# Kernel tuning notes

Measured on AMD Instinct MI355X. Metric: run time of the kernel, lower is better.

The kernel has to match this reference:

```python
import jax, jax.numpy as jnp
import numpy as np

N_NODES = 50000
N_EDGES = 1_600_000
IN_DIM = 512
HIDDEN = 512
OUT_DIM = 128
K = 10
ALPHA = 0.1


def setup_inputs() -> dict:
    key = jax.random.key(0)
    ks = jax.random.split(key, 7)
    x = jax.random.normal(ks[0], (N_NODES, IN_DIM), dtype=jnp.float32)
    edge_index = jax.random.randint(ks[1], (2, N_EDGES), 0, N_NODES, dtype=jnp.int64)
    s_in = 1.0 / np.sqrt(IN_DIM)
    s_h = 1.0 / np.sqrt(HIDDEN)
    lin_in_w = jax.random.uniform(ks[2], (HIDDEN, IN_DIM), jnp.float32, -s_in, s_in)
    lin_in_b = jax.random.uniform(ks[3], (HIDDEN,), jnp.float32, -s_in, s_in)
    lin_out_w = jax.random.uniform(ks[4], (OUT_DIM, HIDDEN), jnp.float32, -s_h, s_h)
    lin_out_b = jax.random.uniform(ks[5], (OUT_DIM,), jnp.float32, -s_h, s_h)
    # GPR init: alpha*(1-alpha)^k, normalized
    w = np.array([ALPHA * (1 - ALPHA) ** k for k in range(K + 1)], dtype=np.float32)
    gpr_weights = jnp.asarray(w / w.sum())
    return {
        "x": x, "edge_index": edge_index,
        "lin_in_w": lin_in_w, "lin_in_b": lin_in_b,
        "lin_out_w": lin_out_w, "lin_out_b": lin_out_b,
        "gpr_weights": gpr_weights,
    }


def reference(x, edge_index, lin_in_w, lin_in_b, lin_out_w, lin_out_b, gpr_weights):
    n = x.shape[0]
    loops = jnp.arange(n, dtype=edge_index.dtype)
    row = jnp.concatenate([edge_index[0], loops])  # [E+n]
    col = jnp.concatenate([edge_index[1], loops])
    # degree over rows (edge_index_sl[0]), clamped to >=1
    deg = jax.ops.segment_sum(jnp.ones_like(row, dtype=x.dtype), row, num_segments=n)
    dis = jnp.clip(deg, 1.0) ** -0.5  # deg^-0.5, [n]

    h = jax.nn.relu(x @ lin_in_w.T + lin_in_b)  # [n, hidden] (dropout = identity in eval)
    w = jax.nn.softmax(gpr_weights)  # [K+1]

    def step(carry, wk):
        h_prop, acc = carry
        hs = h_prop * dis[:, None]
        h_prop = jax.ops.segment_sum(hs[col], row, num_segments=n) * dis[:, None]
        return (h_prop, acc + wk * h_prop), None

    (_, h_final), _ = jax.lax.scan(step, (h, w[0] * h), w[1:])
    return h_final @ lin_out_w.T + lin_out_b
```

## Files before the change

### kernel.cpp

```cpp
#include <hip/hip_runtime.h>


#define SLOTS 96
#define CAP 2688

typedef __attribute__((ext_vector_type(8))) short short8;
typedef __attribute__((ext_vector_type(4))) float f32x4;

__device__ inline ushort f2bf(float f) {
    uint x = __float_as_uint(f);
    return (ushort)((x + 0x7fffu + ((x >> 16) & 1u)) >> 16);
}
__device__ inline float bflo(uint u) { return __uint_as_float(u << 16); }
__device__ inline float bfhi(uint u) { return __uint_as_float(u & 0xffff0000u); }

__global__ void init_misc_kernel(int* __restrict__ bcur, int nbc,
                                 ushort* __restrict__ yAll, size_t ystride, int zrow) {
    int i = blockIdx.x * blockDim.x + threadIdx.x;
    int stride = gridDim.x * blockDim.x;
    for (int j = i; j < nbc; j += stride) bcur[j] = 0;
    for (int j = i; j < 11 * 128; j += stride) {
        int k = j >> 7, d = j & 127;
        yAll[(size_t)k * ystride + (size_t)zrow * 128 + d] = 0;
    }
}

__global__ void fill_u32_kernel(uint* __restrict__ p, uint v, int cnt) {
    int i = blockIdx.x * blockDim.x + threadIdx.x;
    int stride = gridDim.x * blockDim.x;
    for (; i < cnt; i += stride) p[i] = v;
}

__global__ void bucket_scatter_kernel(const int* __restrict__ row, const int* __restrict__ col,
                                      int* __restrict__ bcur, uint* __restrict__ bbuf, int E) {
    int i = blockIdx.x * blockDim.x + threadIdx.x;
    int stride = gridDim.x * blockDim.x;
    for (; i < E; i += stride) {
        int r = __builtin_nontemporal_load(&row[i]);
        int c = __builtin_nontemporal_load(&col[i]);
        int b = r >> 6;
        int pos = atomicAdd(&bcur[b * 16], 1);
        if (pos < CAP)
            bbuf[(size_t)b * CAP + pos] = ((uint)(r & 63) << 16) | (uint)c;
    }
}

__global__ __launch_bounds__(256) void bucket_expand_kernel(
    const int* __restrict__ bcur, const uint* __restrict__ bbuf,
    ushort* __restrict__ col_s, int* __restrict__ deg,
    float* __restrict__ dis, float* __restrict__ dis2, float* __restrict__ rdis, int n) {
    __shared__ int cur[64];
    const int tid = threadIdx.x;
    const int b = blockIdx.x;
    if (tid < 64) cur[tid] = 0;
    __syncthreads();
    int cb = bcur[b * 16];
    if (cb > CAP) cb = CAP;
    const size_t bb = (size_t)b * CAP;
    for (int i = tid; i < cb; i += 256) {
        uint e = bbuf[bb + i];
        int rl = (int)(e >> 16);
        int pos = atomicAdd(&cur[rl], 1);
        if (pos < SLOTS)
            col_s[((size_t)(b * 64 + rl)) * SLOTS + pos] = (ushort)(e & 0xffffu);
    }
    __syncthreads();
    if (tid < 64) {
        int r = b * 64 + tid;
        if (r < n) {
            int d = cur[tid];
            deg[r] = d;
            float fd = (float)(d + 1);
            float di = rsqrtf(fd);
            dis[r] = di;
            dis2[r] = di * di;
            rdis[r] = sqrtf(fd);
        }
    }
}

__global__ void cvt_bf16_kernel(const float* __restrict__ in, ushort* __restrict__ out, int n4) {
    int i = blockIdx.x * blockDim.x + threadIdx.x;
    int stride = gridDim.x * blockDim.x;
    const float4* I = reinterpret_cast<const float4*>(in);
    ushort4* O = reinterpret_cast<ushort4*>(out);
    for (; i < n4; i += stride) {
        float4 v = I[i];
        ushort4 o;
        o.x = f2bf(v.x); o.y = f2bf(v.y); o.z = f2bf(v.z); o.w = f2bf(v.w);
        O[i] = o;
    }
}

template <int EPI>
__global__ __launch_bounds__(256) void gemm_mfma_kernel(
    const void* __restrict__ Ap, const ushort* __restrict__ B,
    const float* __restrict__ bias, const float* __restrict__ dis,
    ushort* __restrict__ outH, int M, int N, int K) {
    __shared__ __align__(16) short As[128 * 32];
    __shared__ __align__(16) short Bs[128 * 32];
    const int tid = threadIdx.x;
    const int lane = tid & 63;
    const int wv = tid >> 6;
    const int wm = (wv >> 1) * 64;
    const int wn = (wv & 1) * 64;
    const int bm = blockIdx.y * 128;
    const int bn = blockIdx.x * 128;
    const int lrow = lane & 15;
    const int lk8 = (lane >> 4) * 8;

    f32x4 acc[4][4];
#pragma unroll
    for (int i = 0; i < 4; ++i)
#pragma unroll
        for (int j = 0; j < 4; ++j) acc[i][j] = (f32x4)(0.f);

    const int r0 = tid >> 2;
    const int g0 = (tid & 3) * 8;

    for (int k0 = 0; k0 < K; k0 += 32) {
        short8 a0, a1;
        if (EPI == 0) {
            const float* Af = (const float*)Ap;
            float4 f0 = make_float4(0.f, 0.f, 0.f, 0.f), f1 = f0, f2 = f0, f3 = f0;
            if (bm + r0 < M) {
                f0 = *reinterpret_cast<const float4*>(Af + (size_t)(bm + r0) * K + k0 + g0);
                f1 = *reinterpret_cast<const float4*>(Af + (size_t)(bm + r0) * K + k0 + g0 + 4);
            }
            if (bm + r0 + 64 < M) {
                f2 = *reinterpret_cast<const float4*>(Af + (size_t)(bm + r0 + 64) * K + k0 + g0);
                f3 = *reinterpret_cast<const float4*>(Af + (size_t)(bm + r0 + 64) * K + k0 + g0 + 4);
            }
            a0[0] = (short)f2bf(f0.x); a0[1] = (short)f2bf(f0.y);
            a0[2] = (short)f2bf(f0.z); a0[3] = (short)f2bf(f0.w);
            a0[4] = (short)f2bf(f1.x); a0[5] = (short)f2bf(f1.y);
            a0[6] = (short)f2bf(f1.z); a0[7] = (short)f2bf(f1.w);
            a1[0] = (short)f2bf(f2.x); a1[1] = (short)f2bf(f2.y);
            a1[2] = (short)f2bf(f2.z); a1[3] = (short)f2bf(f2.w);
            a1[4] = (short)f2bf(f3.x); a1[5] = (short)f2bf(f3.y);
            a1[6] = (short)f2bf(f3.z); a1[7] = (short)f2bf(f3.w);
        } else {
            const ushort* Ab = (const ushort*)Ap;
            a0 = *reinterpret_cast<const short8*>(Ab + (size_t)(bm + r0) * K + k0 + g0);
            a1 = *reinterpret_cast<const short8*>(Ab + (size_t)(bm + r0 + 64) * K + k0 + g0);
        }
        short8 b0 = *reinterpret_cast<const short8*>(B + (size_t)(bn + r0) * K + k0 + g0);
        short8 b1 = *reinterpret_cast<const short8*>(B + (size_t)(bn + r0 + 64) * K + k0 + g0);
        __syncthreads();
        *reinterpret_cast<short8*>(As + r0 * 32 + g0) = a0;
        *reinterpret_cast<short8*>(As + (r0 + 64) * 32 + g0) = a1;
        *reinterpret_cast<short8*>(Bs + r0 * 32 + g0) = b0;
        *reinterpret_cast<short8*>(Bs + (r0 + 64) * 32 + g0) = b1;
        __syncthreads();
        short8 af[4], bfr[4];
#pragma unroll
        for (int mf = 0; mf < 4; ++mf)
            af[mf] = *reinterpret_cast<const short8*>(As + (wm + mf * 16 + lrow) * 32 + lk8);
#pragma unroll
        for (int nf = 0; nf < 4; ++nf)
            bfr[nf] = *reinterpret_cast<const short8*>(Bs + (wn + nf * 16 + lrow) * 32 + lk8);
#pragma unroll
        for (int mf = 0; mf < 4; ++mf)
#pragma unroll
            for (int nf = 0; nf < 4; ++nf)
                acc[mf][nf] = __builtin_amdgcn_mfma_f32_16x16x32_bf16(af[mf], bfr[nf], acc[mf][nf], 0, 0, 0);
    }

#pragma unroll
    for (int mf = 0; mf < 4; ++mf) {
#pragma unroll
        for (int nf = 0; nf < 4; ++nf) {
            const int col = bn + wn + nf * 16 + lrow;
#pragma unroll
            for (int r = 0; r < 4; ++r) {
                const int row = bm + wm + mf * 16 + (lane >> 4) * 4 + r;
                if (row < M) {
                    float v = acc[mf][nf][r];
                    if (EPI == 0) {
                        v = fmaxf(v + bias[col], 0.f);
                        outH[(size_t)row * N + col] = f2bf(v);
                    } else {
                        outH[(size_t)row * N + col] = f2bf(dis[row] * v);
                    }
                }
            }
        }
    }
}

__global__ __launch_bounds__(256) void spmm128_kernel(
    const int* __restrict__ deg, const ushort* __restrict__ col_s,
    const float* __restrict__ dis2,
    const ushort* __restrict__ y_old, ushort* __restrict__ y_new, int n) {
    int wid = (blockIdx.x * 256 + threadIdx.x) >> 6;
    if (wid >= n) return;
    wid = __builtin_amdgcn_readfirstlane(wid);
    const int lane = threadIdx.x & 63;
    int cnt = deg[wid];
    if (cnt > SLOTS) cnt = SLOTS;
    const int cnt16 = (cnt + 15) & ~15;
    const ushort* __restrict__ cp = col_s + (size_t)wid * SLOTS;
    const uint* __restrict__ Y = reinterpret_cast<const uint*>(y_old);
    float s0a = 0.f, s1a = 0.f, s0b = 0.f, s1b = 0.f;
    for (int t = 0; t < cnt16; t += 16) {
        int c[16];
        uint v[16];
#pragma unroll
        for (int j = 0; j < 16; ++j) c[j] = (int)cp[t + j];
#pragma unroll
        for (int j = 0; j < 16; ++j) v[j] = Y[(size_t)c[j] * 64 + lane];
#pragma unroll
        for (int j = 0; j < 16; ++j) {
            if (j & 1) { s0b += bflo(v[j]); s1b += bfhi(v[j]); }
            else       { s0a += bflo(v[j]); s1a += bfhi(v[j]); }
        }
    }
    const uint u = Y[(size_t)wid * 64 + lane];
    const float d2 = dis2[wid];
    const float y0 = d2 * (bflo(u) + (s0a + s0b));
    const float y1 = d2 * (bfhi(u) + (s1a + s1b));
    const uint pv = (uint)f2bf(y0) | ((uint)f2bf(y1) << 16);
    __builtin_nontemporal_store(pv, &reinterpret_cast<uint*>(y_new)[(size_t)wid * 64 + lane]);
}

__global__ __launch_bounds__(256) void finsum_kernel(
    const ushort* __restrict__ yAll, size_t ystride_dw,
    const float* __restrict__ gpr, const float* __restrict__ rdis,
    const float* __restrict__ bout, float* __restrict__ outp, int n) {
    __shared__ float w[11];
    if (threadIdx.x == 0) {
        float m = gpr[0];
        for (int i = 1; i < 11; ++i) m = fmaxf(m, gpr[i]);
        float e[11], s = 0.f;
        for (int i = 0; i < 11; ++i) { e[i] = expf(gpr[i] - m); s += e[i]; }
        float inv = 1.f / s;
        for (int i = 0; i < 11; ++i) w[i] = e[i] * inv;
    }
    __syncthreads();
    const int gid = blockIdx.x * 256 + threadIdx.x;
    if (gid >= n * 64) return;
    const int row = gid >> 6;
    const int lane = gid & 63;
    const uint* __restrict__ Y = reinterpret_cast<const uint*>(yAll);
    float s0 = 0.f, s1 = 0.f;
#pragma unroll
    for (int k = 0; k < 11; ++k) {
        const uint v = Y[k * ystride_dw + (size_t)row * 64 + lane];
        const float wk = w[k];
        s0 = fmaf(wk, bflo(v), s0);
        s1 = fmaf(wk, bfhi(v), s1);
    }
    const float r = rdis[row];
    float2 o;
    o.x = fmaf(s0, r, bout[lane * 2 + 0]);
    o.y = fmaf(s1, r, bout[lane * 2 + 1]);
    *reinterpret_cast<float2*>(outp + (size_t)row * 128 + lane * 2) = o;
}

extern "C" void kernel_launch(void* const* d_in, const int* in_sizes, int n_in,
                              void* d_out, int out_size, void* d_ws, size_t ws_size,
                              hipStream_t stream) {
    const float* x    = (const float*)d_in[0];
    const int*   ei   = (const int*)d_in[1];
    const float* win  = (const float*)d_in[2];
    const float* bin  = (const float*)d_in[3];
    const float* wout = (const float*)d_in[4];
    const float* bout = (const float*)d_in[5];
    const float* gpr  = (const float*)d_in[6];
    float* out = (float*)d_out;

    const int n = in_sizes[0] / 512;
    const int E = in_sizes[1] / 2;
    const int Mpad = ((n + 127) / 128) * 128;
    const int nb = (n + 63) >> 6;

    char* ws = (char*)d_ws;
    size_t off = 0;
    auto take = [&](size_t bytes) -> char* {
        char* p = ws + off;
        off += (bytes + 511) & ~(size_t)511;
        return p;
    };
    int*    deg     = (int*)take((size_t)n * sizeof(int));
    float*  dis     = (float*)take((size_t)n * sizeof(float));
    float*  dis2    = (float*)take((size_t)n * sizeof(float));
    float*  rdis    = (float*)take((size_t)n * sizeof(float));
    int*    bcur    = (int*)take((size_t)nb * 16 * sizeof(int));
    uint*   bbuf    = (uint*)take((size_t)nb * CAP * sizeof(uint));
    ushort* col_s   = (ushort*)take((size_t)n * SLOTS * sizeof(ushort));
    ushort* win_bf  = (ushort*)take((size_t)512 * 512 * sizeof(ushort));
    ushort* wout_bf = (ushort*)take((size_t)128 * 512 * sizeof(ushort));
    ushort* h_bf    = (ushort*)take((size_t)Mpad * 512 * sizeof(ushort));
    const size_t ystride = (size_t)Mpad * 128;
    ushort* yAll    = (ushort*)take(11 * ystride * sizeof(ushort));

    const int* rowp = ei;
    const int* colp = ei + E;

    init_misc_kernel<<<64, 256, 0, stream>>>(bcur, nb * 16, yAll, ystride, n);
    fill_u32_kernel<<<2048, 256, 0, stream>>>(
        (uint*)col_s, ((uint)n << 16) | (uint)n, n * SLOTS / 2);
    bucket_scatter_kernel<<<2048, 256, 0, stream>>>(rowp, colp, bcur, bbuf, E);
    bucket_expand_kernel<<<nb, 256, 0, stream>>>(bcur, bbuf, col_s, deg, dis, dis2, rdis, n);

    cvt_bf16_kernel<<<256, 256, 0, stream>>>(win, win_bf, 512 * 128);
    cvt_bf16_kernel<<<64, 256, 0, stream>>>(wout, wout_bf, 128 * 128);

    dim3 g1(4, Mpad / 128);
    gemm_mfma_kernel<0><<<g1, 256, 0, stream>>>(x, win_bf, bin, nullptr, h_bf, n, 512, 512);

    dim3 g2(1, Mpad / 128);
    gemm_mfma_kernel<2><<<g2, 256, 0, stream>>>(h_bf, wout_bf, nullptr, dis, yAll, n, 128, 512);

    const int spmm_blocks = (n + 3) / 4;
    for (int k = 1; k <= 10; ++k) {
        spmm128_kernel<<<spmm_blocks, 256, 0, stream>>>(
            deg, col_s, dis2, yAll + (size_t)(k - 1) * ystride, yAll + (size_t)k * ystride, n);
    }

    finsum_kernel<<<(n * 64 + 255) / 256, 256, 0, stream>>>(
        yAll, ystride / 2, gpr, rdis, bout, out, n);
}
```

Measured before the change: 738.1 us.

## Fuse weight bf16 conversion into GEMMs, merge init kernels, pad LDS, widen GEMM1 tile

Removes the separate bf16 conversion kernels for the weights; both GEMMs now read fp32 weights and convert them while staging into shared memory. The two init/fill kernels are merged into one launch. Shared-memory rows are padded from 32 to 36 shorts to cut bank conflicts on fragment loads. GEMM1 is split out with a 128x256 tile and 512 threads, which halves how often x is reloaded across N tiles, in exchange for converting the weights redundantly in every block.

Result: faster. 721.8 us (-2.2%).

```diff
diff --git a/kernel.cpp b/kernel.cpp
--- a/kernel.cpp
+++ b/kernel.cpp
@@ -3,6 +3,7 @@
 
 #define SLOTS 96
 #define CAP 2688
+#define LDP 36
 
 typedef __attribute__((ext_vector_type(8))) short short8;
 typedef __attribute__((ext_vector_type(4))) float f32x4;
@@ -14,21 +15,26 @@
 __device__ inline float bflo(uint u) { return __uint_as_float(u << 16); }
 __device__ inline float bfhi(uint u) { return __uint_as_float(u & 0xffff0000u); }
 
-__global__ void init_misc_kernel(int* __restrict__ bcur, int nbc,
-                                 ushort* __restrict__ yAll, size_t ystride, int zrow) {
-    int i = blockIdx.x * blockDim.x + threadIdx.x;
-    int stride = gridDim.x * blockDim.x;
-    for (int j = i; j < nbc; j += stride) bcur[j] = 0;
-    for (int j = i; j < 11 * 128; j += stride) {
-        int k = j >> 7, d = j & 127;
+__device__ inline short8 pack8(float4 a, float4 b) {
+    short8 o;
+    o[0] = (short)f2bf(a.x); o[1] = (short)f2bf(a.y);
+    o[2] = (short)f2bf(a.z); o[3] = (short)f2bf(a.w);
+    o[4] = (short)f2bf(b.x); o[5] = (short)f2bf(b.y);
+    o[6] = (short)f2bf(b.z); o[7] = (short)f2bf(b.w);
+    return o;
+}
+
+__global__ void init_kernel(int* __restrict__ bcur, int nbc,
+                            ushort* __restrict__ yAll, size_t ystride, int zrow,
+                            uint* __restrict__ cfill, int cfcnt, uint cfval) {
+    const int gid = blockIdx.x * blockDim.x + threadIdx.x;
+    const int stride = gridDim.x * blockDim.x;
+    for (int i = gid; i < cfcnt; i += stride) cfill[i] = cfval;
+    for (int i = gid; i < nbc; i += stride) bcur[i] = 0;
+    for (int i = gid; i < 11 * 128; i += stride) {
+        int k = i >> 7, d = i & 127;
         yAll[(size_t)k * ystride + (size_t)zrow * 128 + d] = 0;
     }
-}
-
-__global__ void fill_u32_kernel(uint* __restrict__ p, uint v, int cnt) {
-    int i = blockIdx.x * blockDim.x + threadIdx.x;
-    int stride = gridDim.x * blockDim.x;
-    for (; i < cnt; i += stride) p[i] = v;
 }
 
 __global__ void bucket_scatter_kernel(const int* __restrict__ row, const int* __restrict__ col,
@@ -79,33 +85,95 @@
     }
 }
 
-__global__ void cvt_bf16_kernel(const float* __restrict__ in, ushort* __restrict__ out, int n4) {
-    int i = blockIdx.x * blockDim.x + threadIdx.x;
-    int stride = gridDim.x * blockDim.x;
-    const float4* I = reinterpret_cast<const float4*>(in);
-    ushort4* O = reinterpret_cast<ushort4*>(out);
-    for (; i < n4; i += stride) {
-        float4 v = I[i];
-        ushort4 o;
-        o.x = f2bf(v.x); o.y = f2bf(v.y); o.z = f2bf(v.z); o.w = f2bf(v.w);
-        O[i] = o;
-    }
-}
-
-template <int EPI>
-__global__ __launch_bounds__(256) void gemm_mfma_kernel(
-    const void* __restrict__ Ap, const ushort* __restrict__ B,
-    const float* __restrict__ bias, const float* __restrict__ dis,
-    ushort* __restrict__ outH, int M, int N, int K) {
-    __shared__ __align__(16) short As[128 * 32];
-    __shared__ __align__(16) short Bs[128 * 32];
+__global__ __launch_bounds__(512) void gemm1_kernel(
+    const float* __restrict__ X, const float* __restrict__ Wf,
+    const float* __restrict__ bias, ushort* __restrict__ outH, int M) {
+    __shared__ __align__(16) short As[128 * LDP];
+    __shared__ __align__(16) short Bs[256 * LDP];
+    const int tid = threadIdx.x;
+    const int lane = tid & 63;
+    const int wv = tid >> 6;
+    const int wm = (wv >> 2) * 64;
+    const int wn = (wv & 3) * 64;
+    const int bm = blockIdx.y * 128;
+    const int bn = blockIdx.x * 256;
+    const int lrow = lane & 15;
+    const int lk8 = (lane >> 4) * 8;
+
+    f32x4 acc[4][4];
+#pragma unroll
+    for (int i = 0; i < 4; ++i)
+#pragma unroll
+        for (int j = 0; j < 4; ++j) acc[i][j] = (f32x4)(0.f);
+
+    const int ra = tid >> 2;
+    const int ga = (tid & 3) * 8;
+    const int rb = tid >> 1;
+    const int gb = (tid & 1) * 16;
+
+    for (int k0 = 0; k0 < 512; k0 += 32) {
+        float4 fz = make_float4(0.f, 0.f, 0.f, 0.f);
+        float4 f0 = fz, f1 = fz;
+        if (bm + ra < M) {
+            const float* xp = X + (size_t)(bm + ra) * 512 + k0 + ga;
+            f0 = *reinterpret_cast<const float4*>(xp);
+            f1 = *reinterpret_cast<const float4*>(xp + 4);
+        }
+        short8 av = pack8(f0, f1);
+        const float* wp = Wf + (size_t)(bn + rb) * 512 + k0 + gb;
+        float4 g0 = *reinterpret_cast<const float4*>(wp);
+        float4 g1 = *reinterpret_cast<const float4*>(wp + 4);
+        float4 g2 = *reinterpret_cast<const float4*>(wp + 8);
+        float4 g3 = *reinterpret_cast<const float4*>(wp + 12);
+        short8 bv0 = pack8(g0, g1);
+        short8 bv1 = pack8(g2, g3);
+        __syncthreads();
+        *reinterpret_cast<short8*>(As + ra * LDP + ga) = av;
+        *reinterpret_cast<short8*>(Bs + rb * LDP + gb) = bv0;
+        *reinterpret_cast<short8*>(Bs + rb * LDP + gb + 8) = bv1;
+        __syncthreads();
+        short8 af[4], bfr[4];
+#pragma unroll
+        for (int mf = 0; mf < 4; ++mf)
+            af[mf] = *reinterpret_cast<const short8*>(As + (wm + mf * 16 + lrow) * LDP + lk8);
+#pragma unroll
+        for (int nf = 0; nf < 4; ++nf)
+            bfr[nf] = *reinterpret_cast<const short8*>(Bs + (wn + nf * 16 + lrow) * LDP + lk8);
+#pragma unroll
+        for (int mf = 0; mf < 4; ++mf)
+#pragma unroll
+            for (int nf = 0; nf < 4; ++nf)
+                acc[mf][nf] = __builtin_amdgcn_mfma_f32_16x16x32_bf16(af[mf], bfr[nf], acc[mf][nf], 0, 0, 0);
+    }
+
+#pragma unroll
+    for (int mf = 0; mf < 4; ++mf) {
+#pragma unroll
+        for (int nf = 0; nf < 4; ++nf) {
+            const int col = bn + wn + nf * 16 + lrow;
+#pragma unroll
+            for (int r = 0; r < 4; ++r) {
+                const int row = bm + wm + mf * 16 + (lane >> 4) * 4 + r;
+                if (row < M) {
+                    float v = fmaxf(acc[mf][nf][r] + bias[col], 0.f);
+                    outH[(size_t)row * 512 + col] = f2bf(v);
+                }
+            }
+        }
+    }
+}
+
+__global__ __launch_bounds__(256) void gemm2_kernel(
+    const ushort* __restrict__ H, const float* __restrict__ Wf,
+    const float* __restrict__ dis, ushort* __restrict__ outY, int M) {
+    __shared__ __align__(16) short As[128 * LDP];
+    __shared__ __align__(16) short Bs[128 * LDP];
     const int tid = threadIdx.x;
     const int lane = tid & 63;
     const int wv = tid >> 6;
     const int wm = (wv >> 1) * 64;
     const int wn = (wv & 1) * 64;
-    const int bm = blockIdx.y * 128;
-    const int bn = blockIdx.x * 128;
+    const int bm = blockIdx.x * 128;
     const int lrow = lane & 15;
     const int lk8 = (lane >> 4) * 8;
 
@@ -115,50 +183,34 @@
 #pragma unroll
         for (int j = 0; j < 4; ++j) acc[i][j] = (f32x4)(0.f);
 
-    const int r0 = tid >> 2;
-    const int g0 = (tid & 3) * 8;
-
-    for (int k0 = 0; k0 < K; k0 += 32) {
-        short8 a0, a1;
-        if (EPI == 0) {
-            const float* Af = (const float*)Ap;
-            float4 f0 = make_float4(0.f, 0.f, 0.f, 0.f), f1 = f0, f2 = f0, f3 = f0;
-            if (bm + r0 < M) {
-                f0 = *reinterpret_cast<const float4*>(Af + (size_t)(bm + r0) * K + k0 + g0);
-                f1 = *reinterpret_cast<const float4*>(Af + (size_t)(bm + r0) * K + k0 + g0 + 4);
-            }
-            if (bm + r0 + 64 < M) {
-                f2 = *reinterpret_cast<const float4*>(Af + (size_t)(bm + r0 + 64) * K + k0 + g0);
-                f3 = *reinterpret_cast<const float4*>(Af + (size_t)(bm + r0 + 64) * K + k0 + g0 + 4);
-            }
-            a0[0] = (short)f2bf(f0.x); a0[1] = (short)f2bf(f0.y);
-            a0[2] = (short)f2bf(f0.z); a0[3] = (short)f2bf(f0.w);
-            a0[4] = (short)f2bf(f1.x); a0[5] = (short)f2bf(f1.y);
-            a0[6] = (short)f2bf(f1.z); a0[7] = (short)f2bf(f1.w);
-            a1[0] = (short)f2bf(f2.x); a1[1] = (short)f2bf(f2.y);
-            a1[2] = (short)f2bf(f2.z); a1[3] = (short)f2bf(f2.w);
-            a1[4] = (short)f2bf(f3.x); a1[5] = (short)f2bf(f3.y);
-            a1[6] = (short)f2bf(f3.z); a1[7] = (short)f2bf(f3.w);
-        } else {
-            const ushort* Ab = (const ushort*)Ap;
-            a0 = *reinterpret_cast<const short8*>(Ab + (size_t)(bm + r0) * K + k0 + g0);
-            a1 = *reinterpret_cast<const short8*>(Ab + (size_t)(bm + r0 + 64) * K + k0 + g0);
-        }
-        short8 b0 = *reinterpret_cast<const short8*>(B + (size_t)(bn + r0) * K + k0 + g0);
-        short8 b1 = *reinterpret_cast<const short8*>(B + (size_t)(bn + r0 + 64) * K + k0 + g0);
+    const int ra = tid >> 2;
+    const int ga = (tid & 3) * 8;
+    const int rb = tid >> 1;
+    const int gb = (tid & 1) * 16;
+
+    for (int k0 = 0; k0 < 512; k0 += 32) {
+        short8 a0 = *reinterpret_cast<const short8*>(H + (size_t)(bm + ra) * 512 + k0 + ga);
+        short8 a1 = *reinterpret_cast<const short8*>(H + (size_t)(bm + ra + 64) * 512 + k0 + ga);
+        const float* wp = Wf + (size_t)rb * 512 + k0 + gb;
+        float4 g0 = *reinterpret_cast<const float4*>(wp);
+        float4 g1 = *reinterpret_cast<const float4*>(wp + 4);
+        float4 g2 = *reinterpret_cast<const float4*>(wp + 8);
+        float4 g3 = *reinterpret_cast<const float4*>(wp + 12);
+        short8 bv0 = pack8(g0, g1);
+        short8 bv1 = pack8(g2, g3);
         __syncthreads();
-        *reinterpret_cast<short8*>(As + r0 * 32 + g0) = a0;
-        *reinterpret_cast<short8*>(As + (r0 + 64) * 32 + g0) = a1;
-        *reinterpret_cast<short8*>(Bs + r0 * 32 + g0) = b0;
-        *reinterpret_cast<short8*>(Bs + (r0 + 64) * 32 + g0) = b1;
+        *reinterpret_cast<short8*>(As + ra * LDP + ga) = a0;
+        *reinterpret_cast<short8*>(As + (ra + 64) * LDP + ga) = a1;
+        *reinterpret_cast<short8*>(Bs + rb * LDP + gb) = bv0;
+        *reinterpret_cast<short8*>(Bs + rb * LDP + gb + 8) = bv1;
         __syncthreads();
         short8 af[4], bfr[4];
 #pragma unroll
         for (int mf = 0; mf < 4; ++mf)
-            af[mf] = *reinterpret_cast<const short8*>(As + (wm + mf * 16 + lrow) * 32 + lk8);
+            af[mf] = *reinterpret_cast<const short8*>(As + (wm + mf * 16 + lrow) * LDP + lk8);
 #pragma unroll
         for (int nf = 0; nf < 4; ++nf)
-            bfr[nf] = *reinterpret_cast<const short8*>(Bs + (wn + nf * 16 + lrow) * 32 + lk8);
+            bfr[nf] = *reinterpret_cast<const short8*>(Bs + (wn + nf * 16 + lrow) * LDP + lk8);
 #pragma unroll
         for (int mf = 0; mf < 4; ++mf)
 #pragma unroll
@@ -170,19 +222,12 @@
     for (int mf = 0; mf < 4; ++mf) {
 #pragma unroll
         for (int nf = 0; nf < 4; ++nf) {
-            const int col = bn + wn + nf * 16 + lrow;
+            const int col = wn + nf * 16 + lrow;
 #pragma unroll
             for (int r = 0; r < 4; ++r) {
                 const int row = bm + wm + mf * 16 + (lane >> 4) * 4 + r;
-                if (row < M) {
-                    float v = acc[mf][nf][r];
-                    if (EPI == 0) {
-                        v = fmaxf(v + bias[col], 0.f);
-                        outH[(size_t)row * N + col] = f2bf(v);
-                    } else {
-                        outH[(size_t)row * N + col] = f2bf(dis[row] * v);
-                    }
-                }
+                if (row < M)
+                    outY[(size_t)row * 128 + col] = f2bf(dis[row] * acc[mf][nf][r]);
             }
         }
     }
@@ -288,8 +333,6 @@
     int*    bcur    = (int*)take((size_t)nb * 16 * sizeof(int));
     uint*   bbuf    = (uint*)take((size_t)nb * CAP * sizeof(uint));
     ushort* col_s   = (ushort*)take((size_t)n * SLOTS * sizeof(ushort));
-    ushort* win_bf  = (ushort*)take((size_t)512 * 512 * sizeof(ushort));
-    ushort* wout_bf = (ushort*)take((size_t)128 * 512 * sizeof(ushort));
     ushort* h_bf    = (ushort*)take((size_t)Mpad * 512 * sizeof(ushort));
     const size_t ystride = (size_t)Mpad * 128;
     ushort* yAll    = (ushort*)take(11 * ystride * sizeof(ushort));
@@ -297,20 +340,16 @@
     const int* rowp = ei;
     const int* colp = ei + E;
 
-    init_misc_kernel<<<64, 256, 0, stream>>>(bcur, nb * 16, yAll, ystride, n);
-    fill_u32_kernel<<<2048, 256, 0, stream>>>(
-        (uint*)col_s, ((uint)n << 16) | (uint)n, n * SLOTS / 2);
+    init_kernel<<<2048, 256, 0, stream>>>(bcur, nb * 16, yAll, ystride, n,
+                                          (uint*)col_s, n * SLOTS / 2,
+                                          ((uint)n << 16) | (uint)n);
     bucket_scatter_kernel<<<2048, 256, 0, stream>>>(rowp, colp, bcur, bbuf, E);
     bucket_expand_kernel<<<nb, 256, 0, stream>>>(bcur, bbuf, col_s, deg, dis, dis2, rdis, n);
 
-    cvt_bf16_kernel<<<256, 256, 0, stream>>>(win, win_bf, 512 * 128);
-    cvt_bf16_kernel<<<64, 256, 0, stream>>>(wout, wout_bf, 128 * 128);
-
-    dim3 g1(4, Mpad / 128);
-    gemm_mfma_kernel<0><<<g1, 256, 0, stream>>>(x, win_bf, bin, nullptr, h_bf, n, 512, 512);
-
-    dim3 g2(1, Mpad / 128);
-    gemm_mfma_kernel<2><<<g2, 256, 0, stream>>>(h_bf, wout_bf, nullptr, dis, yAll, n, 128, 512);
+    dim3 g1(2, Mpad / 128);
+    gemm1_kernel<<<g1, 512, 0, stream>>>(x, win, bin, h_bf, n);
+
+    gemm2_kernel<<<Mpad / 128, 256, 0, stream>>>(h_bf, wout, dis, yAll, n);
 
     const int spmm_blocks = (n + 3) / 4;
     for (int k = 1; k <= 10; ++k) {
```
